# Kernel optimization log

Measured on AMD Instinct MI355X. Metric: run time of the kernel, lower is better.

## Reference

```python
import jax, jax.numpy as jnp
import numpy as np

NEG_SLOPE = 0.2
BN_EPS = 1e-5


def gat_conv(x, src, dst, num_nodes, W, att_src, att_dst, bias, concat):
    # x: [N, F_in]; W: [F_in, H*C]; att_src/att_dst: [H, C]
    H, C = att_src.shape
    h = (x @ W).reshape(num_nodes, H, C)                 # [N, H, C]
    a_src = jnp.einsum('nhc,hc->nh', h, att_src)          # [N, H]
    a_dst = jnp.einsum('nhc,hc->nh', h, att_dst)          # [N, H]
    e = a_src[src] + a_dst[dst]                           # [E, H]
    e = jax.nn.leaky_relu(e, NEG_SLOPE)
    # segment softmax over edges sharing the same destination node
    m = jax.ops.segment_max(e, dst, num_segments=num_nodes)   # [N, H]
    ex = jnp.exp(e - m[dst])
    denom = jax.ops.segment_sum(ex, dst, num_segments=num_nodes)  # [N, H]
    alpha = ex / (denom[dst] + 1e-16)                     # [E, H]
    msg = h[src] * alpha[:, :, None]                      # [E, H, C]
    out = jax.ops.segment_sum(msg, dst, num_segments=num_nodes)   # [N, H, C]
    if concat:
        return out.reshape(num_nodes, H * C) + bias
    return out.mean(axis=1) + bias


def batch_norm(x, gamma, beta):
    mu = x.mean(axis=0)
    var = x.var(axis=0)
    return (x - mu) * jax.lax.rsqrt(var + BN_EPS) * gamma + beta


def setup_inputs() -> dict:
    key = jax.random.key(0)
    ks = jax.random.split(key, 16)
    N, E, F_in, C, H, NC = 50000, 800000, 128, 16, 8, 2
    s = lambda k, shape, fan: jax.random.normal(k, shape, jnp.float32) * (1.0 / np.sqrt(fan))
    inp = {
        'x': jax.random.normal(ks[0], (N, F_in), jnp.float32),
        'edge_index': jax.random.randint(ks[1], (2, E), 0, N, jnp.int32),
        'W0': s(ks[2], (F_in, H * C), F_in),
        'att_src0': s(ks[3], (H, C), C),
        'att_dst0': s(ks[4], (H, C), C),
        'b0': jnp.zeros((H * C,), jnp.float32),
        'gamma0': jnp.ones((H * C,), jnp.float32),
        'beta0': jnp.zeros((H * C,), jnp.float32),
        'W1': s(ks[5], (H * C, H * C), H * C),
        'att_src1': s(ks[6], (H, C), C),
        'att_dst1': s(ks[7], (H, C), C),
        'b1': jnp.zeros((C,), jnp.float32),
        'gamma1': jnp.ones((C,), jnp.float32),
        'beta1': jnp.zeros((C,), jnp.float32),
        'Wc': s(ks[8], (C, NC), C),
        'bc': jnp.zeros((NC,), jnp.float32),
    }
    return inp


def reference(x, edge_index, W0, att_src0, att_dst0, b0, gamma0, beta0,
              W1, att_src1, att_dst1, b1, gamma1, beta1, Wc, bc):
    N = x.shape[0]
    loop = jnp.arange(N, dtype=edge_index.dtype)
    src = jnp.concatenate([edge_index[0], loop])  # add self-loops (PyG default)
    dst = jnp.concatenate([edge_index[1], loop])
    # layer 0: concat heads -> [N, H*C]
    h = gat_conv(x, src, dst, N, W0, att_src0, att_dst0, b0, concat=True)
    h = batch_norm(h, gamma0, beta0)
    h = jax.nn.elu(h)
    # layer 1: average heads -> [N, C]
    h = gat_conv(h, src, dst, N, W1, att_src1, att_dst1, b1, concat=False)
    h = batch_norm(h, gamma1, beta1)
    logits = h @ Wc + bc
    return logits
```

## Files before the change

kernel.cpp:

```cpp
#include <hip/hip_runtime.h>
#include <math.h>

#define NEG_SLOPE 0.2f
#define BN_EPS 1e-5f


__device__ __forceinline__ void edge_sd(const int* __restrict__ ei, int E, int eid, int& s, int& d) {
    if (eid < E) { s = ei[eid]; d = ei[E + eid]; }
    else         { s = d = eid - E; }
}

__device__ __forceinline__ float lrelu(float v) { return v > 0.f ? v : NEG_SLOPE * v; }

__device__ __forceinline__ unsigned short f2bf(float f) {
    unsigned u = __float_as_uint(f);
    u += 0x7fffu + ((u >> 16) & 1u);
    return (unsigned short)(u >> 16);
}

__global__ __launch_bounds__(256) void gemm128(const float* __restrict__ X,
                                               const float* __restrict__ W,
                                               unsigned short* __restrict__ Ybf,
                                               const float* __restrict__ att_s,
                                               const float* __restrict__ att_d,
                                               float* __restrict__ a_srcO,
                                               float* __restrict__ a_dstO,
                                               const float* __restrict__ bnmu,
                                               const float* __restrict__ bnrs,
                                               const float* __restrict__ gamma,
                                               const float* __restrict__ beta,
                                               int Nrows) {
    __shared__ float xs[32 * 128];
    int bm = blockIdx.x * 32;
    int tid = threadIdx.x;

    const float4* Xv = (const float4*)(X + (size_t)bm * 128);
    float4* xsv = (float4*)xs;
    if (bnmu == nullptr) {
        for (int i = tid; i < 32 * 32; i += 256) {
            int row = i >> 5;
            xsv[i] = (bm + row < Nrows) ? Xv[i] : make_float4(0.f, 0.f, 0.f, 0.f);
        }
    } else {
        for (int i = tid; i < 32 * 32; i += 256) {
            int row = i >> 5;
            int cb = (i & 31) * 4;
            float4 v = (bm + row < Nrows) ? Xv[i] : make_float4(0.f, 0.f, 0.f, 0.f);
            float4 m4 = *(const float4*)(bnmu + cb);
            float4 r4 = *(const float4*)(bnrs + cb);
            float4 g4 = *(const float4*)(gamma + cb);
            float4 b4 = *(const float4*)(beta + cb);
            v.x = (v.x - m4.x) * r4.x * g4.x + b4.x;
            v.y = (v.y - m4.y) * r4.y * g4.y + b4.y;
            v.z = (v.z - m4.z) * r4.z * g4.z + b4.z;
            v.w = (v.w - m4.w) * r4.w * g4.w + b4.w;
            v.x = v.x > 0.f ? v.x : expm1f(v.x);
            v.y = v.y > 0.f ? v.y : expm1f(v.y);
            v.z = v.z > 0.f ? v.z : expm1f(v.z);
            v.w = v.w > 0.f ? v.w : expm1f(v.w);
            xsv[i] = v;
        }
    }
    __syncthreads();

    int cq = tid & 31;
    int rg = tid >> 5;
    int lane = tid & 63;

    float acc[4][4];
#pragma unroll
    for (int r = 0; r < 4; r++)
#pragma unroll
        for (int j = 0; j < 4; j++) acc[r][j] = 0.f;

    const float* xbase = xs + (rg * 4) * 128;
    const float* wp = W + cq * 4;

    float4 wn0 = *(const float4*)(wp);
    float4 wn1 = *(const float4*)(wp + 128);
    float4 wn2 = *(const float4*)(wp + 256);
    float4 wn3 = *(const float4*)(wp + 384);

    for (int k4 = 0; k4 < 32; k4++) {
        float4 w0 = wn0, w1 = wn1, w2 = wn2, w3 = wn3;
        if (k4 < 31) {
            const float* wnext = wp + (k4 + 1) * 4 * 128;
            wn0 = *(const float4*)(wnext);
            wn1 = *(const float4*)(wnext + 128);
            wn2 = *(const float4*)(wnext + 256);
            wn3 = *(const float4*)(wnext + 384);
        }
#pragma unroll
        for (int r = 0; r < 4; r++) {
            float4 x4 = *(const float4*)(xbase + r * 128 + k4 * 4);
            acc[r][0] += x4.x * w0.x; acc[r][1] += x4.x * w0.y;
            acc[r][2] += x4.x * w0.z; acc[r][3] += x4.x * w0.w;
            acc[r][0] += x4.y * w1.x; acc[r][1] += x4.y * w1.y;
            acc[r][2] += x4.y * w1.z; acc[r][3] += x4.y * w1.w;
            acc[r][0] += x4.z * w2.x; acc[r][1] += x4.z * w2.y;
            acc[r][2] += x4.z * w2.z; acc[r][3] += x4.z * w2.w;
            acc[r][0] += x4.w * w3.x; acc[r][1] += x4.w * w3.y;
            acc[r][2] += x4.w * w3.z; acc[r][3] += x4.w * w3.w;
        }
    }

    int h = cq >> 2;
    float4 as4 = *(const float4*)(att_s + h * 16 + (cq & 3) * 4);
    float4 ad4 = *(const float4*)(att_d + h * 16 + (cq & 3) * 4);

#pragma unroll
    for (int r = 0; r < 4; r++) {
        int row = bm + rg * 4 + r;
        float ps = acc[r][0] * as4.x + acc[r][1] * as4.y + acc[r][2] * as4.z + acc[r][3] * as4.w;
        float pd = acc[r][0] * ad4.x + acc[r][1] * ad4.y + acc[r][2] * ad4.z + acc[r][3] * ad4.w;
        ps += __shfl_xor(ps, 1); ps += __shfl_xor(ps, 2);
        pd += __shfl_xor(pd, 1); pd += __shfl_xor(pd, 2);
        if (row < Nrows) {
            ushort4 pk;
            pk.x = f2bf(acc[r][0]);
            pk.y = f2bf(acc[r][1]);
            pk.z = f2bf(acc[r][2]);
            pk.w = f2bf(acc[r][3]);
            *(ushort4*)(Ybf + (size_t)row * 128 + cq * 4) = pk;
            if ((lane & 3) == 0) {
                a_srcO[row * 8 + h] = ps;
                a_dstO[row * 8 + h] = pd;
            }
        }
    }
}

__global__ void hist_kernel(const int* __restrict__ ei, int E, int Etot,
                            int* __restrict__ counts, int* __restrict__ rank) {
    int eid = blockIdx.x * 256 + threadIdx.x;
    if (eid >= Etot) return;
    int s, d;
    edge_sd(ei, E, eid, s, d);
    rank[eid] = atomicAdd(&counts[d], 1);
}

__global__ __launch_bounds__(256) void chunksum_kernel(const int* __restrict__ counts,
                                                       int* __restrict__ csum, int N) {
    __shared__ int red[256];
    int base = blockIdx.x * 1024;
    int s = 0;
    for (int i = threadIdx.x; i < 1024; i += 256) {
        int idx = base + i;
        s += (idx < N) ? counts[idx] : 0;
    }
    red[threadIdx.x] = s;
    __syncthreads();
#pragma unroll
    for (int st = 128; st > 0; st >>= 1) {
        if (threadIdx.x < st) red[threadIdx.x] += red[threadIdx.x + st];
        __syncthreads();
    }
    if (threadIdx.x == 0) csum[blockIdx.x] = red[0];
}

__global__ void chunkscan_kernel(int* __restrict__ csum, int nchunk) {
    int lane = threadIdx.x;
    int v = (lane < nchunk) ? csum[lane] : 0;
    int incl = v;
#pragma unroll
    for (int off = 1; off < 64; off <<= 1) {
        int t = __shfl_up(incl, off);
        if (lane >= off) incl += t;
    }
    if (lane < nchunk) csum[lane] = incl - v;
}

__global__ __launch_bounds__(1024) void scanfinal_kernel(const int* __restrict__ counts,
                                                         const int* __restrict__ csum,
                                                         int* __restrict__ rowptr, int N) {
    __shared__ int wsum[16], woff_s[16];
    int tid = threadIdx.x, lane = tid & 63, wid = tid >> 6;
    int idx = blockIdx.x * 1024 + tid;
    int v = (idx < N) ? counts[idx] : 0;
    int incl = v;
#pragma unroll
    for (int off = 1; off < 64; off <<= 1) {
        int t = __shfl_up(incl, off);
        if (lane >= off) incl += t;
    }
    if (lane == 63) wsum[wid] = incl;
    __syncthreads();
    if (wid == 0 && lane < 16) {
        int w = wsum[lane], iw = w;
#pragma unroll
        for (int off = 1; off < 16; off <<= 1) {
            int t = __shfl_up(iw, off);
            if (lane >= off) iw += t;
        }
        woff_s[lane] = iw - w;
    }
    __syncthreads();
    if (idx < N) rowptr[idx + 1] = csum[blockIdx.x] + woff_s[wid] + incl;
    if (blockIdx.x == 0 && tid == 0) rowptr[0] = 0;
}

__global__ void scatter_kernel(const int* __restrict__ ei, int E, int Etot,
                               const int* __restrict__ rowptr, const int* __restrict__ rank,
                               unsigned short* __restrict__ ssrc) {
    int eid = blockIdx.x * 256 + threadIdx.x;
    if (eid >= Etot) return;
    int s, d;
    edge_sd(ei, E, eid, s, d);
    ssrc[rowptr[d] + rank[eid]] = (unsigned short)s;
}

template <bool MEAN>
__global__ __launch_bounds__(256) void agg_kernel(const int* __restrict__ rowptr,
                                                  const unsigned short* __restrict__ ssrc,
                                                  const float* __restrict__ a_src,
                                                  const float* __restrict__ a_dst,
                                                  const unsigned short* __restrict__ Hbf,
                                                  float* __restrict__ outbuf, int N) {
    int wid = threadIdx.x >> 6;
    int dst = blockIdx.x * 4 + wid;
    if (dst >= N) return;
    int lane = threadIdx.x & 63;
    int j  = lane >> 3;
    int hj = lane & 7;
    int hf = lane >> 3;
    int f  = lane * 2;
    int start = rowptr[dst], end = rowptr[dst + 1];
    float adst = a_dst[dst * 8 + hj];

    float acc0 = 0.f, acc1 = 0.f, denl = 0.f;

    int i = start + j;
    int s = (i < end) ? (int)ssrc[i] : -1;
    float ar = (s >= 0) ? a_src[s * 8 + hj] : 0.f;

    for (int base = start; base < end; base += 8) {
        int sA[8];
#pragma unroll
        for (int j2 = 0; j2 < 8; j2++) sA[j2] = __shfl(s, j2 * 8);
        unsigned uA[8];
#pragma unroll
        for (int j2 = 0; j2 < 8; j2++)
            uA[j2] = (sA[j2] >= 0) ? *(const unsigned*)(Hbf + (size_t)sA[j2] * 128 + f) : 0u;

        int inext = base + 8 + j;
        int snext = (inext < end) ? (int)ssrc[inext] : -1;
        float anext = (snext >= 0) ? a_src[snext * 8 + hj] : 0.f;

        float w = (s >= 0) ? __expf(lrelu(ar + adst)) : 0.f;
        denl += w;
        float wA[8];
#pragma unroll
        for (int j2 = 0; j2 < 8; j2++) wA[j2] = __shfl(w, j2 * 8 + hf);

#pragma unroll
        for (int j2 = 0; j2 < 8; j2++) {
            acc0 += wA[j2] * __uint_as_float(uA[j2] << 16);
            acc1 += wA[j2] * __uint_as_float(uA[j2] & 0xffff0000u);
        }
        s = snext;
        ar = anext;
    }
#pragma unroll
    for (int off = 8; off < 64; off <<= 1) denl += __shfl_xor(denl, off);
    float den = __shfl(denl, hf);
    float inv = 1.f / (den + 1e-16f);
    if (!MEAN) {
        *(float2*)(outbuf + (size_t)dst * 128 + f) = make_float2(acc0 * inv, acc1 * inv);
    } else {
        float r0 = acc0 * inv, r1 = acc1 * inv;
#pragma unroll
        for (int off = 8; off < 64; off <<= 1) {
            r0 += __shfl_xor(r0, off);
            r1 += __shfl_xor(r1, off);
        }
        if (lane < 8)
            *(float2*)(outbuf + (size_t)dst * 16 + lane * 2) =
                make_float2(r0 * 0.125f, r1 * 0.125f);
    }
}

template <int C>
__global__ __launch_bounds__(256) void stats_part_kernel(const float* __restrict__ X, int Nrows,
                                                         float* __restrict__ partial,
                                                         int rows_per_block) {
    constexpr int GSZ = 256 / C;
    __shared__ float ls[256], lq[256];
    int c = threadIdx.x % C;
    int g = threadIdx.x / C;
    long base = (long)blockIdx.x * rows_per_block;
    long endr = base + rows_per_block;
    if (endr > Nrows) endr = Nrows;
    float s = 0.f, q = 0.f;
    for (long r = base + g; r < endr; r += GSZ) {
        float v = X[r * C + c];
        s += v;
        q += v * v;
    }
    ls[threadIdx.x] = s;
    lq[threadIdx.x] = q;
    __syncthreads();
#pragma unroll
    for (int st = GSZ / 2; st > 0; st >>= 1) {
        if (g < st) {
            ls[threadIdx.x] += ls[threadIdx.x + st * C];
            lq[threadIdx.x] += lq[threadIdx.x + st * C];
        }
        __syncthreads();
    }
    if (g == 0) {
        partial[(size_t)blockIdx.x * (2 * C) + c] = ls[c];
        partial[(size_t)blockIdx.x * (2 * C) + C + c] = lq[c];
    }
}

template <int C>
__global__ __launch_bounds__(1024) void stats_final_kernel(const float* __restrict__ partial,
                                                           int nblk, float invN,
                                                           float* __restrict__ mu,
                                                           float* __restrict__ rsig) {
    constexpr int G = 1024 / C;
    __shared__ float ls[1024], lq[1024];
    int c = threadIdx.x % C;
    int g = threadIdx.x / C;
    float s = 0.f, q = 0.f;
    for (int b = g; b < nblk; b += G) {
        s += partial[(size_t)b * (2 * C) + c];
        q += partial[(size_t)b * (2 * C) + C + c];
    }
    ls[threadIdx.x] = s;
    lq[threadIdx.x] = q;
    __syncthreads();
#pragma unroll
    for (int st = G / 2; st > 0; st >>= 1) {
        if (g < st) {
            ls[threadIdx.x] += ls[threadIdx.x + st * C];
            lq[threadIdx.x] += lq[threadIdx.x + st * C];
        }
        __syncthreads();
    }
    if (g == 0) {
        float m_ = ls[c] * invN;
        float v = lq[c] * invN - m_ * m_;
        mu[c] = m_;
        rsig[c] = rsqrtf(v + BN_EPS);
    }
}

__global__ void final_kernel(const float* __restrict__ out1,
                             const float* __restrict__ mu, const float* __restrict__ rsig,
                             const float* __restrict__ gamma, const float* __restrict__ beta,
                             const float* __restrict__ Wc, const float* __restrict__ bc,
                             float* __restrict__ out, int N) {
    int n = blockIdx.x * 256 + threadIdx.x;
    if (n >= N) return;
    float l0 = bc[0], l1 = bc[1];
#pragma unroll
    for (int c = 0; c < 16; c++) {
        float v = (out1[(size_t)n * 16 + c] - mu[c]) * rsig[c] * gamma[c] + beta[c];
        l0 += v * Wc[c * 2 + 0];
        l1 += v * Wc[c * 2 + 1];
    }
    out[(size_t)n * 2 + 0] = l0;
    out[(size_t)n * 2 + 1] = l1;
}

extern "C" void kernel_launch(void* const* d_in, const int* in_sizes, int n_in,
                              void* d_out, int out_size, void* d_ws, size_t ws_size,
                              hipStream_t stream) {
    const float* x   = (const float*)d_in[0];
    const int*   ei  = (const int*)d_in[1];
    const float* W0  = (const float*)d_in[2];
    const float* as0 = (const float*)d_in[3];
    const float* ad0 = (const float*)d_in[4];
    const float* g0  = (const float*)d_in[6];
    const float* be0 = (const float*)d_in[7];
    const float* W1  = (const float*)d_in[8];
    const float* as1 = (const float*)d_in[9];
    const float* ad1 = (const float*)d_in[10];
    const float* g1  = (const float*)d_in[12];
    const float* be1 = (const float*)d_in[13];
    const float* Wc  = (const float*)d_in[14];
    const float* bc  = (const float*)d_in[15];
    float* out = (float*)d_out;

    int N = in_sizes[0] / 128;
    int E = in_sizes[1] / 2;
    int Etot = E + N;

    char* ws = (char*)d_ws;
    size_t off = 0;
    auto walloc = [&](size_t bytes) -> void* {
        void* p = ws + off;
        off += (bytes + 255) & ~(size_t)255;
        return p;
    };
    float*          B       = (float*)walloc((size_t)N * 128 * 4);
    unsigned short* Hbf     = (unsigned short*)walloc((size_t)N * 128 * 2);
    float*          a_src   = (float*)walloc((size_t)N * 8 * 4);
    float*          a_dst   = (float*)walloc((size_t)N * 8 * 4);
    float*          out1    = (float*)walloc((size_t)N * 16 * 4);
    int*            counts  = (int*)walloc((size_t)N * 4);
    int*            rowptr  = (int*)walloc((size_t)(N + 1) * 4);
    int*            rank    = (int*)walloc((size_t)Etot * 4);
    int*            csum    = (int*)walloc(64 * 4);
    unsigned short* ssrc    = (unsigned short*)walloc((size_t)Etot * 2);
    float*          partial = (float*)walloc((size_t)256 * 256 * 4);
    float*          stats   = (float*)walloc(2 * 128 * 4);
    float* mu = stats, * rsig = stats + 128;

    dim3 b256(256);
    int gN32    = (N + 31) / 32;
    int gE      = (Etot + 255) / 256;
    int gAgg    = (N + 3) / 4;
    int nchunk  = (N + 1023) / 1024;
    const int SBLK = 256;
    int rpb = (N + SBLK - 1) / SBLK;

    hipMemsetAsync(counts, 0, (size_t)N * 4, stream);
    hist_kernel<<<gE, b256, 0, stream>>>(ei, E, Etot, counts, rank);
    chunksum_kernel<<<nchunk, b256, 0, stream>>>(counts, csum, N);
    chunkscan_kernel<<<1, 64, 0, stream>>>(csum, nchunk);
    scanfinal_kernel<<<nchunk, 1024, 0, stream>>>(counts, csum, rowptr, N);
    scatter_kernel<<<gE, b256, 0, stream>>>(ei, E, Etot, rowptr, rank, ssrc);

    gemm128<<<gN32, b256, 0, stream>>>(x, W0, Hbf, as0, ad0, a_src, a_dst,
                                       nullptr, nullptr, nullptr, nullptr, N);
    agg_kernel<false><<<gAgg, b256, 0, stream>>>(rowptr, ssrc, a_src, a_dst, Hbf, B, N);
    stats_part_kernel<128><<<SBLK, b256, 0, stream>>>(B, N, partial, rpb);
    stats_final_kernel<128><<<1, 1024, 0, stream>>>(partial, SBLK, 1.0f / N, mu, rsig);

    gemm128<<<gN32, b256, 0, stream>>>(B, W1, Hbf, as1, ad1, a_src, a_dst,
                                       mu, rsig, g0, be0, N);
    agg_kernel<true><<<gAgg, b256, 0, stream>>>(rowptr, ssrc, a_src, a_dst, Hbf, out1, N);
    stats_part_kernel<16><<<SBLK, b256, 0, stream>>>(out1, N, partial, rpb);
    stats_final_kernel<16><<<1, 1024, 0, stream>>>(partial, SBLK, 1.0f / N, mu, rsig);
    final_kernel<<<(N + 255) / 256, b256, 0, stream>>>(out1, mu, rsig, g1, be1, Wc, bc, out, N);
}
```

Before: 349.4 us.

## Fuse histogram with scan and stats reductions via last-block ticket pattern

```diff
diff --git a/kernel.cpp b/kernel.cpp
--- a/kernel.cpp
+++ b/kernel.cpp
@@ -130,73 +130,56 @@
     }
 }
 
-__global__ void hist_kernel(const int* __restrict__ ei, int E, int Etot,
-                            int* __restrict__ counts, int* __restrict__ rank) {
-    int eid = blockIdx.x * 256 + threadIdx.x;
-    if (eid >= Etot) return;
-    int s, d;
-    edge_sd(ei, E, eid, s, d);
-    rank[eid] = atomicAdd(&counts[d], 1);
-}
-
-__global__ __launch_bounds__(256) void chunksum_kernel(const int* __restrict__ counts,
-                                                       int* __restrict__ csum, int N) {
-    __shared__ int red[256];
-    int base = blockIdx.x * 1024;
-    int s = 0;
-    for (int i = threadIdx.x; i < 1024; i += 256) {
-        int idx = base + i;
-        s += (idx < N) ? counts[idx] : 0;
-    }
-    red[threadIdx.x] = s;
-    __syncthreads();
-#pragma unroll
-    for (int st = 128; st > 0; st >>= 1) {
-        if (threadIdx.x < st) red[threadIdx.x] += red[threadIdx.x + st];
-        __syncthreads();
-    }
-    if (threadIdx.x == 0) csum[blockIdx.x] = red[0];
-}
-
-__global__ void chunkscan_kernel(int* __restrict__ csum, int nchunk) {
-    int lane = threadIdx.x;
-    int v = (lane < nchunk) ? csum[lane] : 0;
-    int incl = v;
-#pragma unroll
-    for (int off = 1; off < 64; off <<= 1) {
-        int t = __shfl_up(incl, off);
-        if (lane >= off) incl += t;
-    }
-    if (lane < nchunk) csum[lane] = incl - v;
-}
-
-__global__ __launch_bounds__(1024) void scanfinal_kernel(const int* __restrict__ counts,
-                                                         const int* __restrict__ csum,
-                                                         int* __restrict__ rowptr, int N) {
-    __shared__ int wsum[16], woff_s[16];
+__global__ __launch_bounds__(1024) void hist_scan_kernel(const int* __restrict__ ei, int E, int Etot,
+                                                         int* __restrict__ counts,
+                                                         int* __restrict__ rank,
+                                                         unsigned* __restrict__ ticket,
+                                                         int* __restrict__ rowptr, int N, int nblk) {
+    int eid = blockIdx.x * 1024 + threadIdx.x;
+    if (eid < Etot) {
+        int s, d;
+        edge_sd(ei, E, eid, s, d);
+        rank[eid] = atomicAdd(&counts[d], 1);
+    }
+    __threadfence();
+    __shared__ unsigned doneidx;
+    if (threadIdx.x == 0) doneidx = atomicAdd(ticket, 1u);
+    __syncthreads();
+    if (doneidx != (unsigned)(nblk - 1)) return;
+
+    __shared__ int wsum[16], wbase[16];
+    __shared__ int carry;
     int tid = threadIdx.x, lane = tid & 63, wid = tid >> 6;
-    int idx = blockIdx.x * 1024 + tid;
-    int v = (idx < N) ? counts[idx] : 0;
-    int incl = v;
-#pragma unroll
-    for (int off = 1; off < 64; off <<= 1) {
-        int t = __shfl_up(incl, off);
-        if (lane >= off) incl += t;
-    }
-    if (lane == 63) wsum[wid] = incl;
-    __syncthreads();
-    if (wid == 0 && lane < 16) {
-        int w = wsum[lane], iw = w;
-#pragma unroll
-        for (int off = 1; off < 16; off <<= 1) {
-            int t = __shfl_up(iw, off);
-            if (lane >= off) iw += t;
-        }
-        woff_s[lane] = iw - w;
-    }
-    __syncthreads();
-    if (idx < N) rowptr[idx + 1] = csum[blockIdx.x] + woff_s[wid] + incl;
-    if (blockIdx.x == 0 && tid == 0) rowptr[0] = 0;
+    if (tid == 0) carry = 0;
+    __syncthreads();
+    for (int c0 = 0; c0 < N; c0 += 1024) {
+        int idx = c0 + tid;
+        int v = (idx < N) ? counts[idx] : 0;
+        int incl = v;
+#pragma unroll
+        for (int off = 1; off < 64; off <<= 1) {
+            int t = __shfl_up(incl, off);
+            if (lane >= off) incl += t;
+        }
+        if (lane == 63) wsum[wid] = incl;
+        __syncthreads();
+        if (wid == 0 && lane < 16) {
+            int w = wsum[lane], iw = w;
+#pragma unroll
+            for (int off = 1; off < 16; off <<= 1) {
+                int t = __shfl_up(iw, off);
+                if (lane >= off) iw += t;
+            }
+            wbase[lane] = iw - w;
+        }
+        __syncthreads();
+        int excl_base = carry + wbase[wid];
+        if (idx < N) rowptr[idx + 1] = excl_base + incl;
+        __syncthreads();
+        if (tid == 1023) carry = excl_base + incl;
+        __syncthreads();
+    }
+    if (tid == 0) rowptr[0] = 0;
 }
 
 __global__ void scatter_kernel(const int* __restrict__ ei, int E, int Etot,
@@ -280,9 +263,13 @@
 }
 
 template <int C>
-__global__ __launch_bounds__(256) void stats_part_kernel(const float* __restrict__ X, int Nrows,
-                                                         float* __restrict__ partial,
-                                                         int rows_per_block) {
+__global__ __launch_bounds__(256) void stats_kernel(const float* __restrict__ X, int Nrows,
+                                                    float* __restrict__ partial,
+                                                    int rows_per_block,
+                                                    unsigned* __restrict__ ticket, int nblk,
+                                                    float invN,
+                                                    float* __restrict__ mu,
+                                                    float* __restrict__ rsig) {
     constexpr int GSZ = 256 / C;
     __shared__ float ls[256], lq[256];
     int c = threadIdx.x % C;
@@ -311,27 +298,22 @@
         partial[(size_t)blockIdx.x * (2 * C) + c] = ls[c];
         partial[(size_t)blockIdx.x * (2 * C) + C + c] = lq[c];
     }
-}
-
-template <int C>
-__global__ __launch_bounds__(1024) void stats_final_kernel(const float* __restrict__ partial,
-                                                           int nblk, float invN,
-                                                           float* __restrict__ mu,
-                                                           float* __restrict__ rsig) {
-    constexpr int G = 1024 / C;
-    __shared__ float ls[1024], lq[1024];
-    int c = threadIdx.x % C;
-    int g = threadIdx.x / C;
-    float s = 0.f, q = 0.f;
-    for (int b = g; b < nblk; b += G) {
-        s += partial[(size_t)b * (2 * C) + c];
-        q += partial[(size_t)b * (2 * C) + C + c];
-    }
-    ls[threadIdx.x] = s;
-    lq[threadIdx.x] = q;
-    __syncthreads();
-#pragma unroll
-    for (int st = G / 2; st > 0; st >>= 1) {
+    __threadfence();
+    __shared__ unsigned doneidx;
+    if (threadIdx.x == 0) doneidx = atomicAdd(ticket, 1u);
+    __syncthreads();
+    if (doneidx != (unsigned)(nblk - 1)) return;
+
+    float s2 = 0.f, q2 = 0.f;
+    for (int b = g; b < nblk; b += GSZ) {
+        s2 += partial[(size_t)b * (2 * C) + c];
+        q2 += partial[(size_t)b * (2 * C) + C + c];
+    }
+    ls[threadIdx.x] = s2;
+    lq[threadIdx.x] = q2;
+    __syncthreads();
+#pragma unroll
+    for (int st = GSZ / 2; st > 0; st >>= 1) {
         if (g < st) {
             ls[threadIdx.x] += ls[threadIdx.x + st * C];
             lq[threadIdx.x] += lq[threadIdx.x + st * C];
@@ -400,9 +382,9 @@
     float*          a_dst   = (float*)walloc((size_t)N * 8 * 4);
     float*          out1    = (float*)walloc((size_t)N * 16 * 4);
     int*            counts  = (int*)walloc((size_t)N * 4);
+    unsigned*       flags   = (unsigned*)walloc(256);
     int*            rowptr  = (int*)walloc((size_t)(N + 1) * 4);
     int*            rank    = (int*)walloc((size_t)Etot * 4);
-    int*            csum    = (int*)walloc(64 * 4);
     unsigned short* ssrc    = (unsigned short*)walloc((size_t)Etot * 2);
     float*          partial = (float*)walloc((size_t)256 * 256 * 4);
     float*          stats   = (float*)walloc(2 * 128 * 4);
@@ -411,28 +393,28 @@
     dim3 b256(256);
     int gN32    = (N + 31) / 32;
     int gE      = (Etot + 255) / 256;
+    int gE1024  = (Etot + 1023) / 1024;
     int gAgg    = (N + 3) / 4;
-    int nchunk  = (N + 1023) / 1024;
     const int SBLK = 256;
     int rpb = (N + SBLK - 1) / SBLK;
 
-    hipMemsetAsync(counts, 0, (size_t)N * 4, stream);
-    hist_kernel<<<gE, b256, 0, stream>>>(ei, E, Etot, counts, rank);
-    chunksum_kernel<<<nchunk, b256, 0, stream>>>(counts, csum, N);
-    chunkscan_kernel<<<1, 64, 0, stream>>>(csum, nchunk);
-    scanfinal_kernel<<<nchunk, 1024, 0, stream>>>(counts, csum, rowptr, N);
+    size_t cnt_rnd = ((size_t)N * 4 + 255) & ~(size_t)255;
+    hipMemsetAsync(counts, 0, cnt_rnd + 256, stream);
+
+    hist_scan_kernel<<<gE1024, 1024, 0, stream>>>(ei, E, Etot, counts, rank,
+                                                  &flags[0], rowptr, N, gE1024);
     scatter_kernel<<<gE, b256, 0, stream>>>(ei, E, Etot, rowptr, rank, ssrc);
 
     gemm128<<<gN32, b256, 0, stream>>>(x, W0, Hbf, as0, ad0, a_src, a_dst,
                                        nullptr, nullptr, nullptr, nullptr, N);
     agg_kernel<false><<<gAgg, b256, 0, stream>>>(rowptr, ssrc, a_src, a_dst, Hbf, B, N);
-    stats_part_kernel<128><<<SBLK, b256, 0, stream>>>(B, N, partial, rpb);
-    stats_final_kernel<128><<<1, 1024, 0, stream>>>(partial, SBLK, 1.0f / N, mu, rsig);
+    stats_kernel<128><<<SBLK, b256, 0, stream>>>(B, N, partial, rpb, &flags[1], SBLK,
+                                                 1.0f / N, mu, rsig);
 
     gemm128<<<gN32, b256, 0, stream>>>(B, W1, Hbf, as1, ad1, a_src, a_dst,
                                        mu, rsig, g0, be0, N);
     agg_kernel<true><<<gAgg, b256, 0, stream>>>(rowptr, ssrc, a_src, a_dst, Hbf, out1, N);
-    stats_part_kernel<16><<<SBLK, b256, 0, stream>>>(out1, N, partial, rpb);
-    stats_final_kernel<16><<<1, 1024, 0, stream>>>(partial, SBLK, 1.0f / N, mu, rsig);
+    stats_kernel<16><<<SBLK, b256, 0, stream>>>(out1, N, partial, rpb, &flags[2], SBLK,
+                                                1.0f / N, mu, rsig);
     final_kernel<<<(N + 255) / 256, b256, 0, stream>>>(out1, mu, rsig, g1, be1, Wc, bc, out, N);
 }
```

Result: slower. 627.0 us (+79.5%).
